# Kernel optimization log

Hardware: AMD Instinct MI355X
Metric: run time of the kernel (lower is better)

## Reference

```python
import jax, jax.numpy as jnp
import numpy as np

HIDDEN = 512

def setup_inputs() -> dict:
    key = jax.random.key(0)
    kx, kq, kk, kv = jax.random.split(key, 4)
    B, S, H = 4, 4096, HIDDEN
    scale = 1.0 / np.sqrt(H)
    x = jax.random.normal(kx, (B, S, H), dtype=jnp.float32)
    # nn.Linear weights are [out, in]; y = x @ W.T
    Wq = jax.random.normal(kq, (H, H), dtype=jnp.float32) * scale
    Wk = jax.random.normal(kk, (H, H), dtype=jnp.float32) * scale
    Wv = jax.random.normal(kv, (H, H), dtype=jnp.float32) * scale
    return {"x": x, "Wq": Wq, "Wk": Wk, "Wv": Wv}

def reference(x, Wq, Wk, Wv):
    H = x.shape[-1]
    q = jnp.einsum('bsh,oh->bso', x, Wq)
    k = jnp.einsum('bsh,oh->bso', x, Wk)
    v = jnp.einsum('bsh,oh->bso', x, Wv)
    scores = jnp.einsum('bqh,bkh->bqk', q, k) / jnp.sqrt(jnp.asarray(H, x.dtype))
    att = jax.nn.softmax(scores, axis=-1)  # max-subtracted softmax, same math as manual version
    return jnp.einsum('bqk,bkh->bqh', att, v)
```

## Files before the change

kernel.cpp:

```cpp
#include <hip/hip_runtime.h>
#include <stdint.h>

typedef unsigned short u16;
typedef __bf16  bf16x8   __attribute__((ext_vector_type(8)));
typedef float   floatx4  __attribute__((ext_vector_type(4)));
typedef unsigned short ushortx4 __attribute__((ext_vector_type(4)));

__device__ __forceinline__ u16 f2bf(float f) {
  unsigned u = __builtin_bit_cast(unsigned, f);
  u += 0x7FFFu + ((u >> 16) & 1u);
  return (u16)(u >> 16);
}

#define GLD_LDS16(g, l)                                                        \
  __builtin_amdgcn_global_load_lds(                                            \
      (const __attribute__((address_space(1))) void*)(g),                      \
      (__attribute__((address_space(3))) void*)(l), 16, 0, 0)

__global__ __launch_bounds__(256) void cvt_w(
    const float* __restrict__ Wq, const float* __restrict__ Wk,
    const float* __restrict__ Wv, u16* __restrict__ dst)
{
  const int z = blockIdx.y;
  const float* src = (z == 0) ? Wq : (z == 1) ? Wk : Wv;
  u16* d = dst + (size_t)z * 262144;
  const int idx = (blockIdx.x * 256 + threadIdx.x) * 8;
  const float4 lo = *(const float4*)&src[idx];
  const float4 hi = *(const float4*)&src[idx + 4];
  union { u16 h[8]; uint4 v; } pk;
  pk.h[0] = f2bf(lo.x); pk.h[1] = f2bf(lo.y); pk.h[2] = f2bf(lo.z); pk.h[3] = f2bf(lo.w);
  pk.h[4] = f2bf(hi.x); pk.h[5] = f2bf(hi.y); pk.h[6] = f2bf(hi.z); pk.h[7] = f2bf(hi.w);
  *(uint4*)&d[idx] = pk.v;
}

__global__ __launch_bounds__(256) void cvt_x(
    const float* __restrict__ X, u16* __restrict__ dst)
{
  const int idx = (blockIdx.x * 256 + threadIdx.x) * 8;
  const float4 lo = *(const float4*)&X[idx];
  const float4 hi = *(const float4*)&X[idx + 4];
  union { u16 h[8]; uint4 v; } pk;
  pk.h[0] = f2bf(lo.x); pk.h[1] = f2bf(lo.y); pk.h[2] = f2bf(lo.z); pk.h[3] = f2bf(lo.w);
  pk.h[4] = f2bf(hi.x); pk.h[5] = f2bf(hi.y); pk.h[6] = f2bf(hi.z); pk.h[7] = f2bf(hi.w);
  *(uint4*)&dst[idx] = pk.v;
}

__global__ __launch_bounds__(256, 2) void qkv_gemm(
    const u16* __restrict__ X16, const u16* __restrict__ Wb,
    u16* __restrict__ qo, u16* __restrict__ ko, u16* __restrict__ vto)
{
  __shared__ u16 As[128 * 32];
  __shared__ u16 Bs[128 * 32];

  const int tid = threadIdx.x;
  const int w  = tid >> 6, l = tid & 63;
  const int lr = l & 15, lq = l >> 4;
  const int lk = lq * 8;
  const int m0 = blockIdx.x * 128;
  const int n0 = blockIdx.y * 128;
  const int z  = blockIdx.z;
  const u16* W = Wb + (size_t)z * 262144;
  const int wm = (w & 1) * 64, wn = (w >> 1) * 64;

  floatx4 acc[4][4];
  const floatx4 fz = {0.f, 0.f, 0.f, 0.f};
#pragma unroll
  for (int i = 0; i < 4; ++i)
#pragma unroll
    for (int j = 0; j < 4; ++j) acc[i][j] = fz;

  for (int kk = 0; kk < 512; kk += 32) {
    __syncthreads();
#pragma unroll
    for (int i = 0; i < 2; ++i) {
      const int c = i * 256 + tid;
      const int row = c >> 2, c8 = (c & 3) * 8;
      GLD_LDS16(X16 + (size_t)(m0 + row) * 512 + kk + c8, &As[c * 8]);
      GLD_LDS16(W   + (size_t)(n0 + row) * 512 + kk + c8, &Bs[c * 8]);
    }
    __syncthreads();

    bf16x8 af[4], bfr[4];
#pragma unroll
    for (int t = 0; t < 4; ++t) {
      af[t]  = *(const bf16x8*)&As[(wm + t * 16 + lr) * 32 + lk];
      bfr[t] = *(const bf16x8*)&Bs[(wn + t * 16 + lr) * 32 + lk];
    }
#pragma unroll
    for (int i = 0; i < 4; ++i)
#pragma unroll
      for (int j = 0; j < 4; ++j)
        acc[i][j] = __builtin_amdgcn_mfma_f32_16x16x32_bf16(af[i], bfr[j],
                                                            acc[i][j], 0, 0, 0);
  }

  const int cr = lq * 4;
  if (z == 2) {
#pragma unroll
    for (int i = 0; i < 4; ++i)
#pragma unroll
      for (int j = 0; j < 4; ++j) {
        const int n = n0 + wn + j * 16 + lr;
        const int m = m0 + wm + i * 16 + cr;
        ushortx4 pk;
#pragma unroll
        for (int r = 0; r < 4; ++r) pk[r] = f2bf(acc[i][j][r]);
        *(ushortx4*)&vto[(size_t)n * 16384 + m] = pk;
      }
  } else {
    u16* dst = (z == 0) ? qo : ko;
    const float sc = (z == 0) ? 0.06375871732f : 1.0f;
#pragma unroll
    for (int i = 0; i < 4; ++i)
#pragma unroll
      for (int j = 0; j < 4; ++j) {
        const int m = m0 + wm + i * 16 + cr;
        const int n = n0 + wn + j * 16 + lr;
#pragma unroll
        for (int r = 0; r < 4; ++r)
          dst[(size_t)(m + r) * 512 + n] = f2bf(acc[i][j][r] * sc);
      }
  }
}

__global__ __launch_bounds__(256, 2) void qk_exp(
    const u16* __restrict__ q, const u16* __restrict__ k,
    u16* __restrict__ S, float* __restrict__ lsum)
{
  __shared__ u16 As[128 * 32];
  __shared__ u16 Bs[128 * 32];

  const int tid = threadIdx.x;
  const int w  = tid >> 6, l = tid & 63;
  const int lr = l & 15, lq = l >> 4;
  const int lk = lq * 8;
  const int m0 = blockIdx.x * 128;
  const int n0 = blockIdx.y * 128;
  const int b  = blockIdx.z;
  const int wm = (w & 1) * 64, wn = (w >> 1) * 64;
  const size_t rb = (size_t)b * 4096;

  floatx4 acc[4][4];
  const floatx4 fz = {0.f, 0.f, 0.f, 0.f};
#pragma unroll
  for (int i = 0; i < 4; ++i)
#pragma unroll
    for (int j = 0; j < 4; ++j) acc[i][j] = fz;

  for (int kk = 0; kk < 512; kk += 32) {
    __syncthreads();
#pragma unroll
    for (int i = 0; i < 2; ++i) {
      const int c = i * 256 + tid;
      const int row = c >> 2, c8 = (c & 3) * 8;
      GLD_LDS16(q + (rb + m0 + row) * 512 + kk + c8, &As[c * 8]);
      GLD_LDS16(k + (rb + n0 + row) * 512 + kk + c8, &Bs[c * 8]);
    }
    __syncthreads();

    bf16x8 af[4], bfr[4];
#pragma unroll
    for (int t = 0; t < 4; ++t) {
      af[t]  = *(const bf16x8*)&As[(wm + t * 16 + lr) * 32 + lk];
      bfr[t] = *(const bf16x8*)&Bs[(wn + t * 16 + lr) * 32 + lk];
    }
#pragma unroll
    for (int i = 0; i < 4; ++i)
#pragma unroll
      for (int j = 0; j < 4; ++j)
        acc[i][j] = __builtin_amdgcn_mfma_f32_16x16x32_bf16(af[i], bfr[j],
                                                            acc[i][j], 0, 0, 0);
  }

  const int cr = lq * 4;
  u16* Sb = S + ((size_t)b << 24);
#pragma unroll
  for (int i = 0; i < 4; ++i) {
    float rs[4] = {0.f, 0.f, 0.f, 0.f};
#pragma unroll
    for (int j = 0; j < 4; ++j) {
      const int m = m0 + wm + i * 16 + cr;
      const int n = n0 + wn + j * 16 + lr;
#pragma unroll
      for (int r = 0; r < 4; ++r) {
        const float p = __builtin_amdgcn_exp2f(acc[i][j][r] - 17.31234049f);
        rs[r] += p;
        Sb[(size_t)(m + r) * 4096 + n] = f2bf(p);
      }
    }
#pragma unroll
    for (int r = 0; r < 4; ++r) {
      float s = rs[r];
      s += __shfl_xor(s, 1, 16);
      s += __shfl_xor(s, 2, 16);
      s += __shfl_xor(s, 4, 16);
      s += __shfl_xor(s, 8, 16);
      if (lr == 0)
        atomicAdd(&lsum[rb + m0 + wm + i * 16 + cr + r], s);
    }
  }
}

__global__ __launch_bounds__(256, 2) void pv(
    const u16* __restrict__ S, const u16* __restrict__ vt,
    const float* __restrict__ lsum, float* __restrict__ out)
{
  __shared__ u16 As[128 * 32];
  __shared__ u16 Bs[128 * 32];

  const int tid = threadIdx.x;
  const int w  = tid >> 6, l = tid & 63;
  const int lr = l & 15, lq = l >> 4;
  const int lk = lq * 8;
  const int m0 = blockIdx.x * 128;
  const int n0 = blockIdx.y * 128;
  const int b  = blockIdx.z;
  const int wm = (w & 1) * 64, wn = (w >> 1) * 64;
  const u16* Sb = S + ((size_t)b << 24);

  floatx4 acc[4][4];
  const floatx4 fz = {0.f, 0.f, 0.f, 0.f};
#pragma unroll
  for (int i = 0; i < 4; ++i)
#pragma unroll
    for (int j = 0; j < 4; ++j) acc[i][j] = fz;

  for (int kk = 0; kk < 4096; kk += 32) {
    __syncthreads();
#pragma unroll
    for (int i = 0; i < 2; ++i) {
      const int c = i * 256 + tid;
      const int row = c >> 2, c8 = (c & 3) * 8;
      GLD_LDS16(Sb + (size_t)(m0 + row) * 4096 + kk + c8, &As[c * 8]);
      GLD_LDS16(vt + (size_t)(n0 + row) * 16384 + b * 4096 + kk + c8, &Bs[c * 8]);
    }
    __syncthreads();

    bf16x8 af[4], bfr[4];
#pragma unroll
    for (int t = 0; t < 4; ++t) {
      af[t]  = *(const bf16x8*)&As[(wm + t * 16 + lr) * 32 + lk];
      bfr[t] = *(const bf16x8*)&Bs[(wn + t * 16 + lr) * 32 + lk];
    }
#pragma unroll
    for (int i = 0; i < 4; ++i)
#pragma unroll
      for (int j = 0; j < 4; ++j)
        acc[i][j] = __builtin_amdgcn_mfma_f32_16x16x32_bf16(af[i], bfr[j],
                                                            acc[i][j], 0, 0, 0);
  }

  const int cr = lq * 4;
#pragma unroll
  for (int i = 0; i < 4; ++i) {
    const int m = m0 + wm + i * 16 + cr;
    float inv[4];
#pragma unroll
    for (int r = 0; r < 4; ++r)
      inv[r] = 1.0f / lsum[(size_t)b * 4096 + m + r];
#pragma unroll
    for (int j = 0; j < 4; ++j) {
      const int n = n0 + wn + j * 16 + lr;
#pragma unroll
      for (int r = 0; r < 4; ++r)
        out[((size_t)b * 4096 + m + r) * 512 + n] = acc[i][j][r] * inv[r];
    }
  }
}

extern "C" void kernel_launch(void* const* d_in, const int* in_sizes, int n_in,
                              void* d_out, int out_size, void* d_ws, size_t ws_size,
                              hipStream_t stream) {
  (void)in_sizes; (void)n_in; (void)out_size; (void)ws_size;
  const float* x  = (const float*)d_in[0];
  const float* Wq = (const float*)d_in[1];
  const float* Wk = (const float*)d_in[2];
  const float* Wv = (const float*)d_in[3];
  float* out = (float*)d_out;
  u16* ws  = (u16*)d_ws;
  u16* qw  = ws;
  u16* kw  = qw + (size_t)16384 * 512;
  u16* vw  = kw + (size_t)16384 * 512;
  u16* x16 = vw + (size_t)16384 * 512;
  u16* wb  = x16 + (size_t)16384 * 512;
  u16* Sp  = wb + (size_t)3 * 262144;
  float* lsum = (float*)(Sp + ((size_t)4 << 24));

  hipMemsetAsync(lsum, 0, 16384 * sizeof(float), stream);
  cvt_w<<<dim3(128, 3), dim3(256), 0, stream>>>(Wq, Wk, Wv, wb);
  cvt_x<<<dim3(4096), dim3(256), 0, stream>>>(x, x16);
  qkv_gemm<<<dim3(128, 4, 3), dim3(256), 0, stream>>>(x16, wb, qw, kw, vw);
  qk_exp<<<dim3(32, 32, 4), dim3(256), 0, stream>>>(qw, kw, Sp, lsum);
  pv<<<dim3(32, 4, 4), dim3(256), 0, stream>>>(Sp, vw, lsum, out);
}
```

Baseline: 330.8 us.

## Transpose QK tile roles for vectorized P stores and remap PV blocks per XCD

In qk_exp the K and Q operands swap MFMA roles, so each lane's four accumulator values lie along consecutive keys. P can then go out as one 8-byte vector store instead of four strided 2-byte stores. Row sums are reduced across lane groups with fewer shuffles and fewer atomics. The PV kernel switches to a 1D grid with a swizzled block index, so blocks sharing the same S rows and batch land on the same XCD for L2 reuse.

```diff
diff --git a/kernel.cpp b/kernel.cpp
--- a/kernel.cpp
+++ b/kernel.cpp
@@ -153,8 +153,8 @@
     for (int i = 0; i < 2; ++i) {
       const int c = i * 256 + tid;
       const int row = c >> 2, c8 = (c & 3) * 8;
-      GLD_LDS16(q + (rb + m0 + row) * 512 + kk + c8, &As[c * 8]);
-      GLD_LDS16(k + (rb + n0 + row) * 512 + kk + c8, &Bs[c * 8]);
+      GLD_LDS16(k + (rb + n0 + row) * 512 + kk + c8, &As[c * 8]);
+      GLD_LDS16(q + (rb + m0 + row) * 512 + kk + c8, &Bs[c * 8]);
     }
     __syncthreads();
 
@@ -174,30 +174,31 @@
 
   const int cr = lq * 4;
   u16* Sb = S + ((size_t)b << 24);
-#pragma unroll
-  for (int i = 0; i < 4; ++i) {
-    float rs[4] = {0.f, 0.f, 0.f, 0.f};
+  float js[4] = {0.f, 0.f, 0.f, 0.f};
+#pragma unroll
+  for (int i = 0; i < 4; ++i)
 #pragma unroll
     for (int j = 0; j < 4; ++j) {
-      const int m = m0 + wm + i * 16 + cr;
-      const int n = n0 + wn + j * 16 + lr;
+      const int key = n0 + wm + i * 16 + cr;
+      const int qr  = m0 + wn + j * 16 + lr;
+      ushortx4 pk;
+      float s4 = 0.f;
 #pragma unroll
       for (int r = 0; r < 4; ++r) {
         const float p = __builtin_amdgcn_exp2f(acc[i][j][r] - 17.31234049f);
-        rs[r] += p;
-        Sb[(size_t)(m + r) * 4096 + n] = f2bf(p);
+        s4 += p;
+        pk[r] = f2bf(p);
       }
-    }
-#pragma unroll
-    for (int r = 0; r < 4; ++r) {
-      float s = rs[r];
-      s += __shfl_xor(s, 1, 16);
-      s += __shfl_xor(s, 2, 16);
-      s += __shfl_xor(s, 4, 16);
-      s += __shfl_xor(s, 8, 16);
-      if (lr == 0)
-        atomicAdd(&lsum[rb + m0 + wm + i * 16 + cr + r], s);
-    }
+      js[j] += s4;
+      *(ushortx4*)&Sb[(size_t)qr * 4096 + key] = pk;
+    }
+#pragma unroll
+  for (int j = 0; j < 4; ++j) {
+    float s = js[j];
+    s += __shfl_xor(s, 16);
+    s += __shfl_xor(s, 32);
+    if (lq == 0)
+      atomicAdd(&lsum[rb + m0 + wn + j * 16 + lr], s);
   }
 }
 
@@ -212,9 +213,12 @@
   const int w  = tid >> 6, l = tid & 63;
   const int lr = l & 15, lq = l >> 4;
   const int lk = lq * 8;
-  const int m0 = blockIdx.x * 128;
-  const int n0 = blockIdx.y * 128;
-  const int b  = blockIdx.z;
+
+  const int wg = blockIdx.x;
+  const int li = (wg & 7) * 64 + (wg >> 3);
+  const int n0 = (li & 3) * 128;
+  const int m0 = ((li >> 2) & 31) * 128;
+  const int b  = li >> 7;
   const int wm = (w & 1) * 64, wn = (w >> 1) * 64;
   const u16* Sb = S + ((size_t)b << 24);
 
@@ -291,5 +295,5 @@
   cvt_x<<<dim3(4096), dim3(256), 0, stream>>>(x, x16);
   qkv_gemm<<<dim3(128, 4, 3), dim3(256), 0, stream>>>(x16, wb, qw, kw, vw);
   qk_exp<<<dim3(32, 32, 4), dim3(256), 0, stream>>>(qw, kw, Sp, lsum);
-  pv<<<dim3(32, 4, 4), dim3(256), 0, stream>>>(Sp, vw, lsum, out);
-}
+  pv<<<dim3(512), dim3(256), 0, stream>>>(Sp, vw, lsum, out);
+}
```

Measured after the change: 310.2 us. 6.2% less time.
